# Optimization experiments

Measured on AMD Instinct MI355X. Metric: run time of the kernel, lower is better.

The kernel has to match this reference:

```python
import jax, jax.numpy as jnp
import numpy as np

MIN_DISTANCE = 1e-07  # min_distance from __init__
N_LEAVES = 16384
WEIGHTS_DIM = 512


def setup_inputs() -> dict:
    key = jax.random.key(0)
    k1, k2, k3 = jax.random.split(key, 3)
    n_nodes = 2 * N_LEAVES - 1  # complete binary tree, heap layout
    x = jax.random.normal(k1, (N_LEAVES, WEIGHTS_DIM), dtype=jnp.float32)
    # per-node AdditionLayer weights (the learnable delta added to parent weights)
    deltas = jax.random.normal(k2, (n_nodes, WEIGHTS_DIM), dtype=jnp.float32) * 0.05
    # per-node heights (increasing toward leaves in expectation; max() guards negatives)
    heights = jax.random.uniform(k3, (n_nodes,), dtype=jnp.float32)
    return {"x": x, "deltas": deltas, "heights": heights}


def reference(x, deltas, heights):
    n_nodes = deltas.shape[0]
    depth = int(np.log2(n_nodes + 1)) - 1  # static
    parent = (np.arange(n_nodes) - 1) // 2  # static heap parents

    # Cumulative weights down the tree, level by level (depth ~14 static iterations).
    # w[node] = sum of deltas along root->node path == curr_weights at that node.
    w_level = deltas[0:1]  # root: zero_vector + delta_root
    for l in range(1, depth + 1):
        start = 2 ** l - 1
        # each parent feeds its two children (left, right) contiguously in heap order
        w_level = jnp.repeat(w_level, 2, axis=0) + deltas[start:start + 2 ** l]
    w_leaves = w_level  # [n_leaves, weights_dim], leaves in left-to-right order

    # Regularizer: curr_weights - input_weights == delta at every node.
    sq = jnp.sum(deltas * deltas, axis=1)  # [n_nodes]
    branch = jnp.maximum(heights[1:] - heights[parent[1:]], MIN_DISTANCE)
    delta_total = sq[0] + jnp.sum(sq[1:] / branch)  # root term undivided (parent is None)

    # Leaf prediction: x[i] @ curr_weights_leaf_i (the 1xN matvec), concatenated over leaves.
    result = jnp.sum(x * w_leaves, axis=1)  # [n_leaves]
    return result, delta_total.reshape(1)
```

## Files before the change

### kernel.cpp

```cpp
#include <hip/hip_runtime.h>


constexpr int   N_LEAVES = 16384;
constexpr int   DIM      = 512;
constexpr float MIN_DIST = 1e-7f;
constexpr int   LPB      = 8;
constexpr int   GRID     = N_LEAVES / LPB;

typedef float v4f __attribute__((ext_vector_type(4)));
typedef float v2f __attribute__((ext_vector_type(2)));

__device__ __forceinline__ float v4dot(v4f a, v4f b) {
    return a.x * b.x + a.y * b.y + a.z * b.z + a.w * b.w;
}
__device__ __forceinline__ float v4sq(v4f a) { return v4dot(a, a); }

__global__ __launch_bounds__(256) void fused_kernel(
        const float* __restrict__ x,
        const float* __restrict__ deltas,
        const float* __restrict__ heights,
        float* __restrict__ out,
        float* __restrict__ partial) {
    __shared__ __align__(16) float wtop[DIM];
    __shared__ float sqred[4];

    const int tid  = threadIdx.x;
    const int lane = tid & 63;
    const int wave = tid >> 6;

    const int b = (int)(((blockIdx.x & 7u) << 8) | (blockIdx.x >> 3));

    const int leaf0 = LPB * b + 2 * wave;
    const int n14_0 = (N_LEAVES - 1) + leaf0;
    const int n14_1 = n14_0 + 1;
    const int n13   = (n14_0 - 1) >> 1;
    const int n12   = (n13 - 1) >> 1;
    const int n11   = (n12 - 1) >> 1;

    v2f acc = {0.0f, 0.0f};
    #pragma unroll
    for (int l = 0; l <= 11; ++l) {
        const int node = ((1 << l) - 1) + (b >> (11 - l));
        acc += ((const v2f*)(deltas + (size_t)node * DIM))[tid];
    }

    v4f ea, ec;
    float escale = 0.0f;
    bool  has_e  = false;
    if (wave == 0 && b < 2047) {
        const v4f* row = (const v4f*)(deltas + (size_t)b * DIM);
        ea = row[lane]; ec = row[lane + 64];
        escale = (b > 0) ? 1.0f / fmaxf(heights[b] - heights[(b - 1) >> 1], MIN_DIST) : 1.0f;
        has_e = true;
    } else if (wave == 1) {
        const int n = 2047 + b;
        const v4f* row = (const v4f*)(deltas + (size_t)n * DIM);
        ea = row[lane]; ec = row[lane + 64];
        escale = 1.0f / fmaxf(heights[n] - heights[(n - 1) >> 1], MIN_DIST);
        has_e = true;
    }

    const v4f* r14_0 = (const v4f*)(deltas + (size_t)n14_0 * DIM);
    const v4f* r14_1 = (const v4f*)(deltas + (size_t)n14_1 * DIM);
    const v4f* r13   = (const v4f*)(deltas + (size_t)n13 * DIM);
    const v4f* r12   = (const v4f*)(deltas + (size_t)n12 * DIM);
    v4f a14_0 = r14_0[lane], c14_0 = r14_0[lane + 64];
    v4f a14_1 = r14_1[lane], c14_1 = r14_1[lane + 64];
    v4f a13   = r13[lane],   c13   = r13[lane + 64];
    v4f a12   = r12[lane],   c12   = r12[lane + 64];

    const v4f* xr0 = (const v4f*)(x + (size_t)leaf0 * DIM);
    const v4f* xr1 = (const v4f*)(x + (size_t)(leaf0 + 1) * DIM);
    v4f xa0 = xr0[lane], xc0 = xr0[lane + 64];
    v4f xa1 = xr1[lane], xc1 = xr1[lane + 64];

    wtop[2 * tid]     = acc.x;
    wtop[2 * tid + 1] = acc.y;

    float sq_acc = 0.0f;
    if (has_e) sq_acc += (v4sq(ea) + v4sq(ec)) * escale;
    if ((wave & 1) == 0) {
        sq_acc += (v4sq(a12) + v4sq(c12)) / fmaxf(heights[n12] - heights[n11], MIN_DIST);
    }
    sq_acc += (v4sq(a13) + v4sq(c13)) / fmaxf(heights[n13] - heights[n12], MIN_DIST);
    sq_acc += (v4sq(a14_0) + v4sq(c14_0)) / fmaxf(heights[n14_0] - heights[n13], MIN_DIST);
    sq_acc += (v4sq(a14_1) + v4sq(c14_1)) / fmaxf(heights[n14_1] - heights[n13], MIN_DIST);
    #pragma unroll
    for (int off = 32; off; off >>= 1) sq_acc += __shfl_xor(sq_acc, off, 64);
    if (lane == 0) sqred[wave] = sq_acc;

    __syncthreads();

    if (tid == 0) partial[b] = sqred[0] + sqred[1] + sqred[2] + sqred[3];

    const v4f t0 = ((const v4f*)wtop)[lane];
    const v4f t1 = ((const v4f*)wtop)[lane + 64];
    v4f base0 = t0 + a12 + a13;
    v4f base1 = t1 + c12 + c13;
    float d0 = v4dot(xa0, base0 + a14_0) + v4dot(xc0, base1 + c14_0);
    float d1 = v4dot(xa1, base0 + a14_1) + v4dot(xc1, base1 + c14_1);
    #pragma unroll
    for (int off = 32; off; off >>= 1) {
        d0 += __shfl_xor(d0, off, 64);
        d1 += __shfl_xor(d1, off, 64);
    }
    if (lane == 0) { out[leaf0] = d0; out[leaf0 + 1] = d1; }
}

__global__ __launch_bounds__(256) void reduce_kernel(
        const float* __restrict__ partial,
        float* __restrict__ out) {
    const int tid = threadIdx.x, lane = tid & 63, wave = tid >> 6;
    const v4f* p = (const v4f*)partial;
    v4f s0 = p[tid];
    v4f s1 = p[tid + 256];
    float s = (s0.x + s0.y + s0.z + s0.w) + (s1.x + s1.y + s1.z + s1.w);
    #pragma unroll
    for (int off = 32; off; off >>= 1) s += __shfl_xor(s, off, 64);
    __shared__ float red[4];
    if (lane == 0) red[wave] = s;
    __syncthreads();
    if (tid == 0) out[N_LEAVES] = red[0] + red[1] + red[2] + red[3];
}

extern "C" void kernel_launch(void* const* d_in, const int* in_sizes, int n_in,
                              void* d_out, int out_size, void* d_ws, size_t ws_size,
                              hipStream_t stream) {
    const float* x       = (const float*)d_in[0];
    const float* deltas  = (const float*)d_in[1];
    const float* heights = (const float*)d_in[2];
    float* out     = (float*)d_out;
    float* partial = (float*)d_ws;

    fused_kernel<<<GRID, 256, 0, stream>>>(x, deltas, heights, out, partial);
    reduce_kernel<<<1, 256, 0, stream>>>(partial, out);
}
```

Before: 119.4 us.

## Process sixteen leaves per block to halve redundant ancestor-path loads

Each block now handles 16 leaves (4 per wave) instead of 8, so the top-of-tree path sum is accumulated over 11 levels per block and shared by twice as many leaves. The per-wave tree indexing is reworked so each wave loads levels 11 and 12, two level-13 nodes and four leaves, and the regularizer work is reassigned to cover the new node ownership. The grid halves and the final reduce reads 1024 partials instead of 2048. This cuts redundant ancestor-row reads and block count, at the cost of more registers per thread and fewer blocks to hide memory latency.

```diff
diff --git a/kernel.cpp b/kernel.cpp
--- a/kernel.cpp
+++ b/kernel.cpp
@@ -4,7 +4,7 @@
 constexpr int   N_LEAVES = 16384;
 constexpr int   DIM      = 512;
 constexpr float MIN_DIST = 1e-7f;
-constexpr int   LPB      = 8;
+constexpr int   LPB      = 16;
 constexpr int   GRID     = N_LEAVES / LPB;
 
 typedef float v4f __attribute__((ext_vector_type(4)));
@@ -28,51 +28,60 @@
     const int lane = tid & 63;
     const int wave = tid >> 6;
 
-    const int b = (int)(((blockIdx.x & 7u) << 8) | (blockIdx.x >> 3));
+    const int b = (int)(((blockIdx.x & 7u) << 7) | (blockIdx.x >> 3));
 
-    const int leaf0 = LPB * b + 2 * wave;
+    const int leaf0 = LPB * b + 4 * wave;
     const int n14_0 = (N_LEAVES - 1) + leaf0;
-    const int n14_1 = n14_0 + 1;
-    const int n13   = (n14_0 - 1) >> 1;
-    const int n12   = (n13 - 1) >> 1;
+    const int n13a  = (n14_0 - 1) >> 1;
+    const int n13b  = n13a + 1;
+    const int n12   = (n13a - 1) >> 1;
     const int n11   = (n12 - 1) >> 1;
+    const int n10   = (n11 - 1) >> 1;
 
     v2f acc = {0.0f, 0.0f};
     #pragma unroll
-    for (int l = 0; l <= 11; ++l) {
-        const int node = ((1 << l) - 1) + (b >> (11 - l));
+    for (int l = 0; l <= 10; ++l) {
+        const int node = ((1 << l) - 1) + (b >> (10 - l));
         acc += ((const v2f*)(deltas + (size_t)node * DIM))[tid];
     }
 
     v4f ea, ec;
     float escale = 0.0f;
     bool  has_e  = false;
-    if (wave == 0 && b < 2047) {
+    if (wave == 0 && b < 1023) {
         const v4f* row = (const v4f*)(deltas + (size_t)b * DIM);
         ea = row[lane]; ec = row[lane + 64];
         escale = (b > 0) ? 1.0f / fmaxf(heights[b] - heights[(b - 1) >> 1], MIN_DIST) : 1.0f;
         has_e = true;
     } else if (wave == 1) {
-        const int n = 2047 + b;
+        const int n = 1023 + b;
         const v4f* row = (const v4f*)(deltas + (size_t)n * DIM);
         ea = row[lane]; ec = row[lane + 64];
         escale = 1.0f / fmaxf(heights[n] - heights[(n - 1) >> 1], MIN_DIST);
         has_e = true;
     }
 
-    const v4f* r14_0 = (const v4f*)(deltas + (size_t)n14_0 * DIM);
-    const v4f* r14_1 = (const v4f*)(deltas + (size_t)n14_1 * DIM);
-    const v4f* r13   = (const v4f*)(deltas + (size_t)n13 * DIM);
-    const v4f* r12   = (const v4f*)(deltas + (size_t)n12 * DIM);
-    v4f a14_0 = r14_0[lane], c14_0 = r14_0[lane + 64];
-    v4f a14_1 = r14_1[lane], c14_1 = r14_1[lane + 64];
-    v4f a13   = r13[lane],   c13   = r13[lane + 64];
-    v4f a12   = r12[lane],   c12   = r12[lane + 64];
+    const v4f* r11  = (const v4f*)(deltas + (size_t)n11 * DIM);
+    const v4f* r12  = (const v4f*)(deltas + (size_t)n12 * DIM);
+    const v4f* r13A = (const v4f*)(deltas + (size_t)n13a * DIM);
+    const v4f* r13B = (const v4f*)(deltas + (size_t)n13b * DIM);
+    v4f a11 = r11[lane],  c11 = r11[lane + 64];
+    v4f a12 = r12[lane],  c12 = r12[lane + 64];
+    v4f a13A = r13A[lane], c13A = r13A[lane + 64];
+    v4f a13B = r13B[lane], c13B = r13B[lane + 64];
+    v4f a14[4], c14[4];
+    #pragma unroll
+    for (int i = 0; i < 4; ++i) {
+        const v4f* r = (const v4f*)(deltas + (size_t)(n14_0 + i) * DIM);
+        a14[i] = r[lane]; c14[i] = r[lane + 64];
+    }
 
-    const v4f* xr0 = (const v4f*)(x + (size_t)leaf0 * DIM);
-    const v4f* xr1 = (const v4f*)(x + (size_t)(leaf0 + 1) * DIM);
-    v4f xa0 = xr0[lane], xc0 = xr0[lane + 64];
-    v4f xa1 = xr1[lane], xc1 = xr1[lane + 64];
+    v4f xa[4], xc[4];
+    #pragma unroll
+    for (int i = 0; i < 4; ++i) {
+        const v4f* r = (const v4f*)(x + (size_t)(leaf0 + i) * DIM);
+        xa[i] = r[lane]; xc[i] = r[lane + 64];
+    }
 
     wtop[2 * tid]     = acc.x;
     wtop[2 * tid + 1] = acc.y;
@@ -80,11 +89,17 @@
     float sq_acc = 0.0f;
     if (has_e) sq_acc += (v4sq(ea) + v4sq(ec)) * escale;
     if ((wave & 1) == 0) {
-        sq_acc += (v4sq(a12) + v4sq(c12)) / fmaxf(heights[n12] - heights[n11], MIN_DIST);
+        sq_acc += (v4sq(a11) + v4sq(c11)) / fmaxf(heights[n11] - heights[n10], MIN_DIST);
     }
-    sq_acc += (v4sq(a13) + v4sq(c13)) / fmaxf(heights[n13] - heights[n12], MIN_DIST);
-    sq_acc += (v4sq(a14_0) + v4sq(c14_0)) / fmaxf(heights[n14_0] - heights[n13], MIN_DIST);
-    sq_acc += (v4sq(a14_1) + v4sq(c14_1)) / fmaxf(heights[n14_1] - heights[n13], MIN_DIST);
+    sq_acc += (v4sq(a12) + v4sq(c12)) / fmaxf(heights[n12] - heights[n11], MIN_DIST);
+    sq_acc += (v4sq(a13A) + v4sq(c13A)) / fmaxf(heights[n13a] - heights[n12], MIN_DIST);
+    sq_acc += (v4sq(a13B) + v4sq(c13B)) / fmaxf(heights[n13b] - heights[n12], MIN_DIST);
+    #pragma unroll
+    for (int i = 0; i < 4; ++i) {
+        const int np = (i < 2) ? n13a : n13b;
+        sq_acc += (v4sq(a14[i]) + v4sq(c14[i]))
+                / fmaxf(heights[n14_0 + i] - heights[np], MIN_DIST);
+    }
     #pragma unroll
     for (int off = 32; off; off >>= 1) sq_acc += __shfl_xor(sq_acc, off, 64);
     if (lane == 0) sqred[wave] = sq_acc;
@@ -95,16 +110,27 @@
 
     const v4f t0 = ((const v4f*)wtop)[lane];
     const v4f t1 = ((const v4f*)wtop)[lane + 64];
-    v4f base0 = t0 + a12 + a13;
-    v4f base1 = t1 + c12 + c13;
-    float d0 = v4dot(xa0, base0 + a14_0) + v4dot(xc0, base1 + c14_0);
-    float d1 = v4dot(xa1, base0 + a14_1) + v4dot(xc1, base1 + c14_1);
+    const v4f base0 = t0 + a11 + a12;
+    const v4f base1 = t1 + c11 + c12;
+    const v4f bA0 = base0 + a13A, bA1 = base1 + c13A;
+    const v4f bB0 = base0 + a13B, bB1 = base1 + c13B;
+    float d0 = v4dot(xa[0], bA0 + a14[0]) + v4dot(xc[0], bA1 + c14[0]);
+    float d1 = v4dot(xa[1], bA0 + a14[1]) + v4dot(xc[1], bA1 + c14[1]);
+    float d2 = v4dot(xa[2], bB0 + a14[2]) + v4dot(xc[2], bB1 + c14[2]);
+    float d3 = v4dot(xa[3], bB0 + a14[3]) + v4dot(xc[3], bB1 + c14[3]);
     #pragma unroll
     for (int off = 32; off; off >>= 1) {
         d0 += __shfl_xor(d0, off, 64);
         d1 += __shfl_xor(d1, off, 64);
+        d2 += __shfl_xor(d2, off, 64);
+        d3 += __shfl_xor(d3, off, 64);
     }
-    if (lane == 0) { out[leaf0] = d0; out[leaf0 + 1] = d1; }
+    if (lane == 0) {
+        out[leaf0]     = d0;
+        out[leaf0 + 1] = d1;
+        out[leaf0 + 2] = d2;
+        out[leaf0 + 3] = d3;
+    }
 }
 
 __global__ __launch_bounds__(256) void reduce_kernel(
@@ -113,8 +139,7 @@
     const int tid = threadIdx.x, lane = tid & 63, wave = tid >> 6;
     const v4f* p = (const v4f*)partial;
     v4f s0 = p[tid];
-    v4f s1 = p[tid + 256];
-    float s = (s0.x + s0.y + s0.z + s0.w) + (s1.x + s1.y + s1.z + s1.w);
+    float s = s0.x + s0.y + s0.z + s0.w;
     #pragma unroll
     for (int off = 32; off; off >>= 1) s += __shfl_xor(s, off, 64);
     __shared__ float red[4];
```

New measurement: 119.4 us. No clear change (+0.0%).
